# Kernel optimization log

Measured on AMD Instinct MI355X. Metric: run time of the kernel, lower is better.

The kernel has to match this reference:

```python
import jax, jax.numpy as jnp
import numpy as np

NUM_USERS = 100000
NUM_ITEMS = 100000
N_NODES = NUM_USERS + NUM_ITEMS
EMB = 64
N_EDGES = 3200000
N_LAYERS = 3


def setup_inputs() -> dict:
    key = jax.random.key(0)
    k1, k2, k3, k4, k5 = jax.random.split(key, 5)
    user_emb = jax.random.normal(k1, (NUM_USERS, EMB), dtype=jnp.float32)
    item_emb = jax.random.normal(k2, (NUM_ITEMS, EMB), dtype=jnp.float32)
    # COO representation of the normalized adjacency norm_adj (values ~ 1/sqrt(d_i d_j))
    edge_row = jax.random.randint(k3, (N_EDGES,), 0, N_NODES, dtype=jnp.int32)
    edge_col = jax.random.randint(k4, (N_EDGES,), 0, N_NODES, dtype=jnp.int32)
    edge_w = jax.random.uniform(k5, (N_EDGES,), dtype=jnp.float32)
    return {"user_emb": user_emb, "item_emb": item_emb, "edge_w": edge_w,
            "edge_row": edge_row, "edge_col": edge_col}


def _spmm(edge_row, edge_col, edge_w, x):
    # y[r] = sum_{e: row[e]==r} w[e] * x[col[e]]  ==  torch.sparse.mm(norm_adj, x)
    msgs = edge_w[:, None] * x[edge_col]  # [n_edges, E]
    return jax.ops.segment_sum(msgs, edge_row, num_segments=N_NODES)


def reference(user_emb, item_emb, edge_w, edge_row, edge_col):
    ego = jnp.concatenate([user_emb, item_emb], axis=0)  # [N, E]
    acc = jnp.zeros_like(ego)
    for _ in range(N_LAYERS):
        ego = _spmm(edge_row, edge_col, edge_w, ego)
        acc = acc + ego
    final = acc / N_LAYERS  # mean over the n_layers propagated embeddings
    user_all = final[:NUM_USERS]
    item_all = final[NUM_USERS:]
    return (user_all, item_all)
```

## Files before the change

kernel.cpp:

```cpp
#include <hip/hip_runtime.h>
#include <hip/hip_bf16.h>


constexpr int NUM_USERS = 100000;
constexpr int NUM_ITEMS = 100000;
constexpr int N_NODES   = NUM_USERS + NUM_ITEMS;
constexpr int EMB       = 64;
constexpr int N_EDGES   = 3200000;

constexpr int BUCK_SHIFT = 8;
constexpr int NBUCK = (N_NODES + 255) >> BUCK_SHIFT;
constexpr int BIN_BLOCK = 1024;
constexpr int EPB = 16384;
constexpr int NBIN_BLOCKS = (N_EDGES + EPB - 1) / EPB;
constexpr int SORT_CAP = 6144;

constexpr int HIST_BLOCKS   = 512;
constexpr int CONCAT_BLOCKS = (N_NODES * 8 + 255) / 256;


__device__ __forceinline__ float bfl(unsigned u) { return __uint_as_float(u << 16); }
__device__ __forceinline__ float bfh(unsigned u) { return __uint_as_float(u & 0xFFFF0000u); }
__device__ __forceinline__ unsigned f2bf(float f) {
    unsigned u = __float_as_uint(f);
    return (u + 0x7FFFu + ((u >> 16) & 1u)) >> 16;
}
__device__ __forceinline__ unsigned pk(float lo, float hi) {
    return f2bf(lo) | (f2bf(hi) << 16);
}


__global__ __launch_bounds__(256) void prep(
    const int* __restrict__ row, int* __restrict__ bcnt,
    const float4* __restrict__ u, const float4* __restrict__ it,
    uint4* __restrict__ ebuf) {
    __shared__ int h[NBUCK];
    if (blockIdx.x < HIST_BLOCKS) {
        for (int i = threadIdx.x; i < NBUCK; i += 256) h[i] = 0;
        __syncthreads();
        int nt = HIST_BLOCKS * 256;
        for (int e = blockIdx.x * 256 + threadIdx.x; e < N_EDGES; e += nt) {
            int r = __builtin_nontemporal_load(&row[e]);
            atomicAdd(&h[r >> BUCK_SHIFT], 1);
        }
        __syncthreads();
        for (int i = threadIdx.x; i < NBUCK; i += 256) {
            int c = h[i];
            if (c) atomicAdd(&bcnt[i], c);
        }
    } else {
        int i = (blockIdx.x - HIST_BLOCKS) * 256 + threadIdx.x;
        if (i >= N_NODES * 8) return;
        const float4* s = (i < NUM_USERS * 8) ? (u + 2 * (size_t)i)
                                              : (it + 2 * ((size_t)i - (size_t)NUM_USERS * 8));
        float4 f0 = s[0], f1 = s[1];
        uint4 o;
        o.x = pk(f0.x, f0.y); o.y = pk(f0.z, f0.w);
        o.z = pk(f1.x, f1.y); o.w = pk(f1.z, f1.w);
        ebuf[i] = o;
    }
}


__global__ __launch_bounds__(1024) void scan_buckets(const int* __restrict__ bcnt,
                                                     int* __restrict__ bbase,
                                                     int* __restrict__ bcursor) {
    __shared__ int lds[1024];
    int t = threadIdx.x;
    int v = (t < NBUCK) ? bcnt[t] : 0;
    lds[t] = v;
    __syncthreads();
    for (int off = 1; off < 1024; off <<= 1) {
        int x = (t >= off) ? lds[t - off] : 0;
        __syncthreads();
        lds[t] += x;
        __syncthreads();
    }
    int excl = lds[t] - v;
    if (t < NBUCK) { bbase[t] = excl; bcursor[t] = excl; }
    if (t == 0) bbase[NBUCK] = N_EDGES;
}

__global__ __launch_bounds__(BIN_BLOCK) void bin_edges(
    const int* __restrict__ row, const int* __restrict__ col,
    const float* __restrict__ w,
    int* __restrict__ bcursor, int2* __restrict__ binned) {
    __shared__ int hcnt[NBUCK];
    __shared__ int hbase[NBUCK];
    int t = threadIdx.x;
    int e0 = blockIdx.x * EPB;
    int e1 = e0 + EPB; if (e1 > N_EDGES) e1 = N_EDGES;

    for (int i = t; i < NBUCK; i += BIN_BLOCK) hcnt[i] = 0;
    __syncthreads();
    for (int e = e0 + t; e < e1; e += BIN_BLOCK) {
        int r = __builtin_nontemporal_load(&row[e]);
        atomicAdd(&hcnt[r >> BUCK_SHIFT], 1);
    }
    __syncthreads();
    for (int i = t; i < NBUCK; i += BIN_BLOCK) {
        int c = hcnt[i];
        hbase[i] = c ? atomicAdd(&bcursor[i], c) : 0;
        hcnt[i] = 0;
    }
    __syncthreads();
    for (int e = e0 + t; e < e1; e += BIN_BLOCK) {
        int r  = row[e];
        int bk = r >> BUCK_SHIFT;
        int rank = atomicAdd(&hcnt[bk], 1);
        int2 rec = make_int2(__builtin_nontemporal_load(&col[e]) | ((r & 255) << 18),
                             __float_as_int(__builtin_nontemporal_load(&w[e])));
        binned[hbase[bk] + rank] = rec;
    }
}

__global__ __launch_bounds__(256) void sort_bucket(
    const int* __restrict__ bbase, const int2* __restrict__ binned,
    int2* __restrict__ sorted, int* __restrict__ row_start) {
    __shared__ int cnt[256];
    __shared__ int sc[256];
    __shared__ int2 buf[SORT_CAP];
    int b = blockIdx.x, t = threadIdx.x;
    int gb = bbase[b];
    int n  = bbase[b + 1] - gb;

    cnt[t] = 0;
    __syncthreads();
    for (int i = t; i < n; i += 256)
        atomicAdd(&cnt[binned[gb + i].x >> 18], 1);
    __syncthreads();

    int v = cnt[t];
    sc[t] = v;
    __syncthreads();
    for (int off = 1; off < 256; off <<= 1) {
        int x = (t >= off) ? sc[t - off] : 0;
        __syncthreads();
        sc[t] += x;
        __syncthreads();
    }
    int excl = sc[t] - v;

    int r = (b << BUCK_SHIFT) + t;
    if (r < N_NODES) row_start[r] = gb + excl;
    if (b == NBUCK - 1 && t == 0) row_start[N_NODES] = N_EDGES;
    __syncthreads();
    cnt[t] = excl;
    __syncthreads();

    for (int i = t; i < n; i += 256) {
        int2 rec = binned[gb + i];
        int rl = rec.x >> 18;
        int k = atomicAdd(&cnt[rl], 1);
        if (k < SORT_CAP)
            buf[k] = make_int2(rec.x & 0x3FFFF, rec.y);
    }
    __syncthreads();
    int m = n < SORT_CAP ? n : SORT_CAP;
    for (int i = t; i < m; i += 256)
        sorted[gb + i] = buf[i];
}


template<bool LAST>
__global__ __launch_bounds__(256) void spmm_bf16(
    const int* __restrict__ row_start, const int2* __restrict__ sorted,
    const uint4* __restrict__ src,
    uint4* __restrict__ y,
    const uint4* __restrict__ y1,
    float4* __restrict__ out)
{
    int r = (blockIdx.x * blockDim.x + threadIdx.x) >> 3;
    int s = threadIdx.x & 7;
    if (r >= N_NODES) return;
    int s0 = row_start[r];
    int s1 = row_start[r + 1];

    float a0 = 0.f, a1 = 0.f, a2 = 0.f, a3 = 0.f;
    float a4 = 0.f, a5 = 0.f, a6 = 0.f, a7 = 0.f;

    for (int base = s0; base < s1; base += 4) {
        int i0 = base;
        int i1 = min(base + 1, N_EDGES - 1);
        int i2 = min(base + 2, N_EDGES - 1);
        int i3 = min(base + 3, N_EDGES - 1);
        int2 e0 = sorted[i0];
        int2 e1 = sorted[i1];
        int2 e2 = sorted[i2];
        int2 e3 = sorted[i3];
        bool v1 = base + 1 < s1, v2 = base + 2 < s1, v3 = base + 3 < s1;
        int   c0 = e0.x;
        int   c1 = v1 ? e1.x : 0;
        int   c2 = v2 ? e2.x : 0;
        int   c3 = v3 ? e3.x : 0;
        float w0 = __int_as_float(e0.y);
        float w1 = v1 ? __int_as_float(e1.y) : 0.f;
        float w2 = v2 ? __int_as_float(e2.y) : 0.f;
        float w3 = v3 ? __int_as_float(e3.y) : 0.f;
        uint4 g0 = src[(size_t)c0 * 8 + s];
        uint4 g1 = src[(size_t)c1 * 8 + s];
        uint4 g2 = src[(size_t)c2 * 8 + s];
        uint4 g3 = src[(size_t)c3 * 8 + s];
#define ACC(vv, wt) \
        a0 = fmaf(wt, bfl(vv.x), a0); a1 = fmaf(wt, bfh(vv.x), a1); \
        a2 = fmaf(wt, bfl(vv.y), a2); a3 = fmaf(wt, bfh(vv.y), a3); \
        a4 = fmaf(wt, bfl(vv.z), a4); a5 = fmaf(wt, bfh(vv.z), a5); \
        a6 = fmaf(wt, bfl(vv.w), a6); a7 = fmaf(wt, bfh(vv.w), a7);
        ACC(g0, w0) ACC(g1, w1) ACC(g2, w2) ACC(g3, w3)
#undef ACC
    }

    if (!LAST) {
        uint4 o;
        o.x = pk(a0, a1); o.y = pk(a2, a3);
        o.z = pk(a4, a5); o.w = pk(a6, a7);
        y[(size_t)r * 8 + s] = o;
    } else {
        uint4 u1 = y1[(size_t)r * 8 + s];
        uint4 u2 = src[(size_t)r * 8 + s];
        constexpr float sc = 1.0f / 3.0f;
        float4 o0, o1;
        o0.x = (a0 + bfl(u1.x) + bfl(u2.x)) * sc;
        o0.y = (a1 + bfh(u1.x) + bfh(u2.x)) * sc;
        o0.z = (a2 + bfl(u1.y) + bfl(u2.y)) * sc;
        o0.w = (a3 + bfh(u1.y) + bfh(u2.y)) * sc;
        o1.x = (a4 + bfl(u1.z) + bfl(u2.z)) * sc;
        o1.y = (a5 + bfh(u1.z) + bfh(u2.z)) * sc;
        o1.z = (a6 + bfl(u1.w) + bfl(u2.w)) * sc;
        o1.w = (a7 + bfh(u1.w) + bfh(u2.w)) * sc;
        size_t ob = (size_t)r * 16 + 2 * s;
        out[ob]     = o0;
        out[ob + 1] = o1;
    }
}


extern "C" void kernel_launch(void* const* d_in, const int* in_sizes, int n_in,
                              void* d_out, int out_size, void* d_ws, size_t ws_size,
                              hipStream_t stream) {
    const float* user_emb = (const float*)d_in[0];
    const float* item_emb = (const float*)d_in[1];
    const float* edge_w   = (const float*)d_in[2];
    const int*   edge_row = (const int*)d_in[3];
    const int*   edge_col = (const int*)d_in[4];

    char* p = (char*)d_ws;
    uint4* ebuf = (uint4*)p;        p += (size_t)N_NODES * 8 * sizeof(uint4);
    uint4* ybuf = (uint4*)p;        p += (size_t)N_NODES * 8 * sizeof(uint4);
    int2*  sorted = (int2*)p;       p += (size_t)N_EDGES * sizeof(int2);
    int*   bcnt = (int*)p;          p += (size_t)NBUCK * sizeof(int);
    int*   bbase = (int*)p;         p += (size_t)(NBUCK + 1) * sizeof(int);
    int*   bcursor = (int*)p;       p += (size_t)NBUCK * sizeof(int);
    int*   row_start = (int*)p;     p += (size_t)(N_NODES + 1) * sizeof(int);
    int2*  binned = (int2*)ybuf;

    hipMemsetAsync(bcnt, 0, (size_t)NBUCK * sizeof(int), stream);

    prep<<<HIST_BLOCKS + CONCAT_BLOCKS, 256, 0, stream>>>(
        edge_row, bcnt, (const float4*)user_emb, (const float4*)item_emb, ebuf);

    scan_buckets<<<1, 1024, 0, stream>>>(bcnt, bbase, bcursor);
    bin_edges<<<NBIN_BLOCKS, BIN_BLOCK, 0, stream>>>(edge_row, edge_col, edge_w,
                                                     bcursor, binned);
    sort_bucket<<<NBUCK, 256, 0, stream>>>(bbase, binned, sorted, row_start);

    int grid = (N_NODES * 8 + 255) / 256;
    spmm_bf16<false><<<grid, 256, 0, stream>>>(row_start, sorted, ebuf, ybuf,
                                               nullptr, nullptr);
    spmm_bf16<false><<<grid, 256, 0, stream>>>(row_start, sorted, ybuf, ebuf,
                                               nullptr, nullptr);
    spmm_bf16<true><<<grid, 256, 0, stream>>>(row_start, sorted, ebuf, nullptr,
                                              ybuf, (float4*)d_out);
}
```

Baseline: 432.3 us.

## Stage binned edges in LDS before coalesced per-bucket global writes

The binning kernel now sorts each block's edges by bucket in shared memory, using a block-local prefix scan over bucket counts. It then copies each bucket's contiguous run to global memory, with eight lanes per bucket. This replaces scattered 8-byte global stores with locally grouped writes to cut write inefficiency. Block size and edges per block are halved so the 64 KB staging buffer fits in LDS, which doubles the block count and the global cursor atomics, and adds an extra scan and barriers.

```diff
diff --git a/kernel.cpp b/kernel.cpp
--- a/kernel.cpp
+++ b/kernel.cpp
@@ -10,8 +10,8 @@
 
 constexpr int BUCK_SHIFT = 8;
 constexpr int NBUCK = (N_NODES + 255) >> BUCK_SHIFT;
-constexpr int BIN_BLOCK = 1024;
-constexpr int EPB = 16384;
+constexpr int BIN_BLOCK = 512;
+constexpr int EPB = 8192;
 constexpr int NBIN_BLOCKS = (N_EDGES + EPB - 1) / EPB;
 constexpr int SORT_CAP = 6144;
 
@@ -85,32 +85,63 @@
     const int* __restrict__ row, const int* __restrict__ col,
     const float* __restrict__ w,
     int* __restrict__ bcursor, int2* __restrict__ binned) {
-    __shared__ int hcnt[NBUCK];
-    __shared__ int hbase[NBUCK];
+    __shared__ int2 stage[EPB];
+    __shared__ int  hcnt[NBUCK];
+    __shared__ int  hbase[NBUCK];
+    __shared__ int  cursor[NBUCK];
+    __shared__ int  lds2[BIN_BLOCK];
     int t = threadIdx.x;
     int e0 = blockIdx.x * EPB;
     int e1 = e0 + EPB; if (e1 > N_EDGES) e1 = N_EDGES;
 
     for (int i = t; i < NBUCK; i += BIN_BLOCK) hcnt[i] = 0;
     __syncthreads();
-    for (int e = e0 + t; e < e1; e += BIN_BLOCK) {
-        int r = __builtin_nontemporal_load(&row[e]);
-        atomicAdd(&hcnt[r >> BUCK_SHIFT], 1);
-    }
-    __syncthreads();
+    for (int e = e0 + t; e < e1; e += BIN_BLOCK)
+        atomicAdd(&hcnt[row[e] >> BUCK_SHIFT], 1);
+    __syncthreads();
+
     for (int i = t; i < NBUCK; i += BIN_BLOCK) {
         int c = hcnt[i];
         hbase[i] = c ? atomicAdd(&bcursor[i], c) : 0;
-        hcnt[i] = 0;
-    }
-    __syncthreads();
+    }
+    int i0 = 2 * t, i1 = 2 * t + 1;
+    int c0 = (i0 < NBUCK) ? hcnt[i0] : 0;
+    int c1 = (i1 < NBUCK) ? hcnt[i1] : 0;
+    lds2[t] = c0 + c1;
+    __syncthreads();
+    for (int off = 1; off < BIN_BLOCK; off <<= 1) {
+        int x = (t >= off) ? lds2[t - off] : 0;
+        __syncthreads();
+        lds2[t] += x;
+        __syncthreads();
+    }
+    int pairExcl = lds2[t] - (c0 + c1);
+    if (i0 < NBUCK) cursor[i0] = pairExcl;
+    if (i1 < NBUCK) cursor[i1] = pairExcl + c0;
+    __syncthreads();
+
     for (int e = e0 + t; e < e1; e += BIN_BLOCK) {
         int r  = row[e];
         int bk = r >> BUCK_SHIFT;
-        int rank = atomicAdd(&hcnt[bk], 1);
-        int2 rec = make_int2(__builtin_nontemporal_load(&col[e]) | ((r & 255) << 18),
-                             __float_as_int(__builtin_nontemporal_load(&w[e])));
-        binned[hbase[bk] + rank] = rec;
+        int pos = atomicAdd(&cursor[bk], 1);
+        stage[pos] = make_int2(__builtin_nontemporal_load(&col[e]) | ((r & 255) << 18),
+                               __float_as_int(__builtin_nontemporal_load(&w[e])));
+    }
+    __syncthreads();
+
+    int wave = t >> 6;
+    int lane = t & 63;
+    int sl   = lane & 7;
+    constexpr int NWAVE = BIN_BLOCK / 64;
+    for (int base = wave * 8; base < NBUCK; base += NWAVE * 8) {
+        int bk = base + (lane >> 3);
+        if (bk < NBUCK) {
+            int c  = hcnt[bk];
+            int st = cursor[bk] - c;
+            int gp = hbase[bk];
+            for (int j = sl; j < c; j += 8)
+                binned[gp + j] = stage[st + j];
+        }
     }
 }
 
```

New measurement: 416.1 us. 3.7% less time.
